# Optimization experiments

Measured on AMD Instinct MI355X. Metric: run time of the kernel, lower is better.

Reference implementation:

```python
import jax, jax.numpy as jnp
import numpy as np

N = 131072   # num_nodes
E = 262144   # events in the batch
D = 128      # memory_dim
R = 128      # raw_msg_dim
T = 32       # time_dim


def setup_inputs() -> dict:
    key = jax.random.key(0)
    ks = jax.random.split(key, 16)
    s = 0.05
    return {
        "memory": jax.random.normal(ks[0], (N, D), jnp.float32) * s,
        "raw_msg": jax.random.normal(ks[1], (E, R), jnp.float32) * s,
        "time_w": jax.random.normal(ks[2], (T,), jnp.float32) * s,
        "time_b": jax.random.normal(ks[3], (T,), jnp.float32) * s,
        "W_msg_s": jax.random.normal(ks[4], (D, 2 * D + R + T), jnp.float32) * s,
        "b_msg_s": jax.random.normal(ks[5], (D,), jnp.float32) * s,
        "W_msg_d": jax.random.normal(ks[6], (D, 2 * D + R + T), jnp.float32) * s,
        "b_msg_d": jax.random.normal(ks[7], (D,), jnp.float32) * s,
        "W_ih": jax.random.normal(ks[8], (3 * D, D), jnp.float32) * s,
        "W_hh": jax.random.normal(ks[9], (3 * D, D), jnp.float32) * s,
        "b_ih": jax.random.normal(ks[10], (3 * D,), jnp.float32) * s,
        "b_hh": jax.random.normal(ks[11], (3 * D,), jnp.float32) * s,
        "src": jax.random.randint(ks[12], (E,), 0, N, jnp.int32),
        "dst": jax.random.randint(ks[13], (E,), 0, N, jnp.int32),
        "t": jax.random.randint(ks[14], (E,), 0, 100000, jnp.int32),
        "last_update": jax.random.randint(ks[15], (N,), 0, 50000, jnp.int32),
    }


def _time_enc(t_rel, time_w, time_b):
    # TimeEncoder: cos(Linear(t)) ; t_rel: [E] float -> [E, T]
    return jnp.cos(t_rel[:, None] * time_w[None, :] + time_b[None, :])


def _message(mem_a, mem_b, raw_msg, t_enc, W, b):
    # message MLP on concat(mem_src, mem_dst, raw_msg, t_enc)
    x = jnp.concatenate([mem_a, mem_b, raw_msg, t_enc], axis=-1)  # [E, 2D+R+T]
    return jax.nn.relu(x @ W.T + b)


def _forward(memory, raw_msg, time_w, time_b, W_msg_s, b_msg_s, W_msg_d, b_msg_d,
             W_ih, W_hh, b_ih, b_hh, src, dst, t, last_update):
    tf = t.astype(jnp.float32)
    lu = last_update.astype(jnp.float32)
    mem_s = memory[src]  # gather [E, D]
    mem_d = memory[dst]

    # source-side messages (stored under key src): t_rel = t - last_update[src]
    t_enc_s = _time_enc(tf - lu[src], time_w, time_b)
    msg_s = _message(mem_s, mem_d, raw_msg, t_enc_s, W_msg_s, b_msg_s)
    # dest-side messages (stored under key dst, src/dst swapped)
    t_enc_d = _time_enc(tf - lu[dst], time_w, time_b)
    msg_d = _message(mem_d, mem_s, raw_msg, t_enc_d, W_msg_d, b_msg_d)

    # scatter mean-aggregate messages onto their owner node
    seg = jnp.concatenate([src, dst], axis=0)          # [2E]
    vals = jnp.concatenate([msg_s, msg_d], axis=0)     # [2E, D]
    sums = jax.ops.segment_sum(vals, seg, num_segments=N)
    cnt = jax.ops.segment_sum(jnp.ones((2 * E,), jnp.float32), seg, num_segments=N)
    aggr = sums / jnp.maximum(cnt, 1.0)[:, None]       # [N, D]

    # GRUCell(aggr, memory)
    gi = aggr @ W_ih.T + b_ih
    gh = memory @ W_hh.T + b_hh
    i_r, i_z, i_n = jnp.split(gi, 3, axis=-1)
    h_r, h_z, h_n = jnp.split(gh, 3, axis=-1)
    r = jax.nn.sigmoid(i_r + h_r)
    z = jax.nn.sigmoid(i_z + h_z)
    n = jnp.tanh(i_n + r * h_n)
    new_memory = (1.0 - z) * n + z * memory

    # scatter-max timestamps (pyg scatter reduce='max' fills empty slots with 0)
    tt = jnp.concatenate([t, t], axis=0)
    seg_max = jax.ops.segment_max(tt, seg, num_segments=N)
    new_last_update = jnp.where(cnt > 0, seg_max, jnp.zeros((), jnp.int32))
    return new_memory, new_last_update


def reference(memory, raw_msg, time_w, time_b, W_msg_s, b_msg_s, W_msg_d, b_msg_d,
              W_ih, W_hh, b_ih, b_hh, src, dst, t, last_update):
    return _forward(memory, raw_msg, time_w, time_b, W_msg_s, b_msg_s, W_msg_d,
                    b_msg_d, W_ih, W_hh, b_ih, b_hh, src, dst, t, last_update)
```

## Files before the change

### kernel.cpp

```cpp
#include <hip/hip_runtime.h>
#include <cstdint>
#include <cstddef>

#define NN 131072
#define EE 262144

typedef __attribute__((ext_vector_type(8))) short bf16x8;
typedef __attribute__((ext_vector_type(4))) float f32x4;

__device__ __forceinline__ unsigned short f2bf(float f) {
    unsigned int u = __builtin_bit_cast(unsigned int, f);
    u += 0x7FFFu + ((u >> 16) & 1u);
    return (unsigned short)(u >> 16);
}
__device__ __forceinline__ float bf2f(unsigned short s) {
    unsigned int u = ((unsigned int)s) << 16;
    return __builtin_bit_cast(float, u);
}
__device__ __forceinline__ float sigmoidf_(float x) { return 1.0f / (1.0f + __expf(-x)); }
__device__ __forceinline__ float tanhf_(float x) {
    float ax = fabsf(x);
    float e = __expf(-2.0f * ax);
    return copysignf((1.0f - e) / (1.0f + e), x);
}
__device__ __forceinline__ bf16x8 pack8(const float* f) {
    bf16x8 o;
#pragma unroll
    for (int i = 0; i < 8; ++i) o[i] = (short)f2bf(f[i]);
    return o;
}

__device__ __forceinline__ float wmsg_val(int n, int k, const float* Ws, const float* Wd) {
    if (n < 128) {
        return (k < 416) ? Ws[n * 416 + k] : 0.0f;
    } else {
        int m = n - 128;
        if (k < 128)       return Wd[m * 416 + 128 + k];
        else if (k < 256)  return Wd[m * 416 + (k - 128)];
        else if (k < 384)  return Wd[m * 416 + k];
        else if (k < 416)  return 0.0f;
        else               return Wd[m * 416 + 384 + (k - 416)];
    }
}
__device__ __forceinline__ float wgru_val(int j, int k, const float* Wih, const float* Whh) {
    if (j < 256)      return (k < 128) ? Wih[j * 128 + k] : Whh[j * 128 + (k - 128)];
    else if (j < 384) return (k < 128) ? Wih[j * 128 + k] : 0.0f;
    else              return (k < 128) ? 0.0f : Whh[(j - 128) * 128 + (k - 128)];
}

__global__ void k_prep_msgfrag(const float* __restrict__ Ws, const float* __restrict__ Wd,
                               const float* __restrict__ bs, const float* __restrict__ bd,
                               unsigned short* __restrict__ Wmf, float* __restrict__ bm) {
    int b = blockIdx.x;
    int c = b >> 4, nt = b & 15;
    int lane = threadIdx.x;
    int col0 = lane & 15, q = lane >> 4;
    int n = nt * 16 + col0;
    float f[8];
#pragma unroll
    for (int j = 0; j < 8; ++j) f[j] = wmsg_val(n, c * 32 + q * 8 + j, Ws, Wd);
    ((bf16x8*)Wmf)[(size_t)b * 64 + lane] = pack8(f);
    if (b == 0)
        for (int i = lane; i < 256; i += 64) bm[i] = (i < 128) ? bs[i] : bd[i - 128];
}

__global__ void k_prep_grufrag(const float* __restrict__ Wih, const float* __restrict__ Whh,
                               const float* __restrict__ bih, const float* __restrict__ bhh,
                               unsigned short* __restrict__ Wgf, float* __restrict__ bg) {
    int b = blockIdx.x;
    int c = b >> 5, nt = b & 31;
    int lane = threadIdx.x;
    int col0 = lane & 15, q = lane >> 4;
    int j0 = nt * 16 + col0;
    float f[8];
#pragma unroll
    for (int j = 0; j < 8; ++j) f[j] = wgru_val(j0, c * 32 + q * 8 + j, Wih, Whh);
    ((bf16x8*)Wgf)[(size_t)b * 64 + lane] = pack8(f);
    if (b == 0)
        for (int i = lane; i < 512; i += 64)
            bg[i] = (i < 256) ? (bih[i] + bhh[i]) : ((i < 384) ? bih[i] : bhh[i - 128]);
}

__global__ void k_memconv(const float* __restrict__ in, unsigned short* __restrict__ outp) {
    int gid = blockIdx.x * 256 + threadIdx.x;
    const float4 v = ((const float4*)in)[gid];
    ushort4 o;
    o.x = f2bf(v.x); o.y = f2bf(v.y); o.z = f2bf(v.z); o.w = f2bf(v.w);
    *(ushort4*)(outp + (size_t)gid * 4) = o;
}

__global__ void k_pre(const int* __restrict__ t, const int* __restrict__ src,
                      const int* __restrict__ dst, const int* __restrict__ lu,
                      float* __restrict__ trel_s, float* __restrict__ trel_d,
                      int* cnt, int* lu_tmp) {
    int e = blockIdx.x * 256 + threadIdx.x;
    int s = src[e], d = dst[e], tv = t[e];
    trel_s[e] = (float)(tv - lu[s]);
    trel_d[e] = (float)(tv - lu[d]);
    atomicAdd(&cnt[s], 1);
    atomicAdd(&cnt[d], 1);
    atomicMax(&lu_tmp[s], tv);
    atomicMax(&lu_tmp[d], tv);
}

__global__ void k_scan1(const int* __restrict__ cnt, int* __restrict__ bsum) {
    __shared__ int red[256];
    int tid = threadIdx.x;
    red[tid] = cnt[blockIdx.x * 256 + tid];
    __syncthreads();
    for (int s = 128; s > 0; s >>= 1) {
        if (tid < s) red[tid] += red[tid + s];
        __syncthreads();
    }
    if (tid == 0) bsum[blockIdx.x] = red[0];
}
__global__ void k_scan2(const int* __restrict__ bsum, int* __restrict__ boff) {
    __shared__ int sb[512];
    int tid = threadIdx.x;
    int v = bsum[tid];
    sb[tid] = v;
    __syncthreads();
    for (int d = 1; d < 512; d <<= 1) {
        int u = (tid >= d) ? sb[tid - d] : 0;
        __syncthreads();
        sb[tid] += u;
        __syncthreads();
    }
    boff[tid] = sb[tid] - v;
}
__global__ void k_scan3(const int* __restrict__ cnt, const int* __restrict__ boff,
                        int* __restrict__ off, int* __restrict__ cursor) {
    __shared__ int sb[256];
    int tid = threadIdx.x;
    int i = blockIdx.x * 256 + tid;
    int v = cnt[i];
    sb[tid] = v;
    __syncthreads();
    for (int d = 1; d < 256; d <<= 1) {
        int u = (tid >= d) ? sb[tid - d] : 0;
        __syncthreads();
        sb[tid] += u;
        __syncthreads();
    }
    int o = boff[blockIdx.x] + sb[tid] - v;
    off[i] = o;
    cursor[i] = o;
}
__global__ void k_fill(const int* __restrict__ src, const int* __restrict__ dst,
                       int* cursor, int* __restrict__ pos2) {
    int e2 = blockIdx.x * 256 + threadIdx.x;
    int node = (e2 < EE) ? src[e2] : dst[e2 - EE];
    pos2[e2] = atomicAdd(&cursor[node], 1);
}

__launch_bounds__(256, 3)
__global__ void k_msg(const unsigned short* __restrict__ memb,
                      const float* __restrict__ raw,
                      const float* __restrict__ trel_s,
                      const float* __restrict__ trel_d,
                      const unsigned short* __restrict__ Wmf,
                      const float* __restrict__ bm,
                      const int* __restrict__ src, const int* __restrict__ dst,
                      const int* __restrict__ pos2,
                      const float* __restrict__ tw, const float* __restrict__ tb,
                      unsigned short* __restrict__ msg) {
    __shared__ int s_idx[64], d_idx[64], s_pos[64], d_pos[64];
    __shared__ float s_tw[32], s_tb[32];
    __shared__ __align__(16) unsigned short As[2][64 * 40];

    const int tid = threadIdx.x;
    const int e0 = blockIdx.x * 64;
    if (tid < 64)        { s_idx[tid] = src[e0 + tid];            s_pos[tid] = pos2[e0 + tid]; }
    else if (tid < 128)  { d_idx[tid - 64] = dst[e0 + tid - 64];  d_pos[tid - 64] = pos2[EE + e0 + tid - 64]; }
    else if (tid < 160)  s_tw[tid - 128] = tw[tid - 128];
    else if (tid < 192)  s_tb[tid - 160] = tb[tid - 160];
    __syncthreads();

    const int lane = tid & 63, w = tid >> 6;
    const int col0 = lane & 15, q = lane >> 4;

    auto stage = [&](int cc) {
        unsigned short* A = As[cc & 1];
        if (cc < 8) {
            int row = tid >> 2, seg = tid & 3;
            int node = (cc < 4) ? s_idx[row] : d_idx[row];
            bf16x8 v = *(const bf16x8*)(memb + (size_t)node * 128 + (cc & 3) * 32 + seg * 8);
            *(bf16x8*)&A[row * 40 + seg * 8] = v;
        } else if (cc < 12) {
#pragma unroll
            for (int i = 0; i < 2; ++i) {
                int lin = tid + 256 * i;
                int row = lin >> 3, seg = lin & 7;
                const float4 v = *(const float4*)(raw + (size_t)(e0 + row) * 128 + (cc - 8) * 32 + seg * 4);
                ushort4 o;
                o.x = f2bf(v.x); o.y = f2bf(v.y); o.z = f2bf(v.z); o.w = f2bf(v.w);
                *(ushort4*)&A[row * 40 + seg * 4] = o;
            }
        } else {
            int row = tid >> 2, quarter = tid & 3;
            float tr = (cc == 12) ? trel_s[e0 + row] : trel_d[e0 + row];
            float f[8];
#pragma unroll
            for (int j2 = 0; j2 < 8; ++j2) {
                int jj = quarter * 8 + j2;
                f[j2] = __cosf(tr * s_tw[jj] + s_tb[jj]);
            }
            *(bf16x8*)&A[row * 40 + quarter * 8] = pack8(f);
        }
    };

    f32x4 acc[4][4];
#pragma unroll
    for (int a = 0; a < 4; ++a)
#pragma unroll
        for (int b = 0; b < 4; ++b)
#pragma unroll
            for (int i = 0; i < 4; ++i) acc[a][b][i] = 0.0f;

    stage(0);
    __syncthreads();

    for (int c = 0; c < 14; ++c) {
        bf16x8 bfr[4];
        const bf16x8* Wc = (const bf16x8*)Wmf + (size_t)c * 16 * 64;
#pragma unroll
        for (int nl = 0; nl < 4; ++nl)
            bfr[nl] = Wc[(w * 4 + nl) * 64 + lane];
        const unsigned short* A = As[c & 1];
        bf16x8 afr[4];
#pragma unroll
        for (int mt = 0; mt < 4; ++mt)
            afr[mt] = *(const bf16x8*)&A[(mt * 16 + col0) * 40 + q * 8];
        if (c < 13) stage(c + 1);
#pragma unroll
        for (int mt = 0; mt < 4; ++mt)
#pragma unroll
            for (int nl = 0; nl < 4; ++nl)
                acc[mt][nl] = __builtin_amdgcn_mfma_f32_16x16x32_bf16(afr[mt], bfr[nl], acc[mt][nl], 0, 0, 0);
        __syncthreads();
    }

    unsigned short* scr = &As[0][0] + w * 1280;
    const bool is_s = (w < 2);
#pragma unroll
    for (int mt = 0; mt < 4; ++mt) {
#pragma unroll
        for (int nl = 0; nl < 4; ++nl) {
            int j = (w * 4 + nl) * 16 + col0;
            float bv = bm[j];
            int gl = nl * 2 + (col0 >> 3);
            int ci = col0 & 7;
#pragma unroll
            for (int r = 0; r < 4; ++r) {
                int rr = q * 4 + r;
                float v = fmaxf(acc[mt][nl][r] + bv, 0.0f);
                scr[rr * 80 + ((gl + rr) & 7) * 8 + ci] = f2bf(v);
            }
        }
        asm volatile("s_waitcnt lgkmcnt(0)" ::: "memory");
        {
            int rr2 = lane & 15, p = lane >> 4;
            int ev = mt * 16 + rr2;
            int pos = is_s ? s_pos[ev] : d_pos[ev];
            bf16x8 v0 = *(const bf16x8*)&scr[rr2 * 80 + (((2 * p)     + rr2) & 7) * 8];
            bf16x8 v1 = *(const bf16x8*)&scr[rr2 * 80 + (((2 * p + 1) + rr2) & 7) * 8];
            unsigned short* dstp = msg + (size_t)pos * 128 + (w & 1) * 64 + p * 16;
            *(bf16x8*)dstp = v0;
            *(bf16x8*)(dstp + 8) = v1;
        }
        asm volatile("s_waitcnt lgkmcnt(0)" ::: "memory");
    }
}

__launch_bounds__(256, 3)
__global__ void k_gru(const unsigned short* __restrict__ msg,
                      const int* __restrict__ off, const int* __restrict__ cnt,
                      const float* __restrict__ memory,
                      const unsigned short* __restrict__ Wgf,
                      const float* __restrict__ bg,
                      float* __restrict__ out) {
    __shared__ __align__(16) unsigned short Xs[32 * 264];

    const int tid = threadIdx.x;
    const int n0 = blockIdx.x * 32;

    {
        int g = tid >> 3, sub = tid & 7;
        int node = n0 + g;
        int beg = off[node], cn = cnt[node];
        float a[16];
#pragma unroll
        for (int i = 0; i < 16; ++i) a[i] = 0.0f;
        for (int m = 0; m < cn; ++m) {
            const bf16x8* p = (const bf16x8*)(msg + (size_t)(beg + m) * 128 + sub * 16);
            bf16x8 v0 = p[0], v1 = p[1];
#pragma unroll
            for (int k = 0; k < 8; ++k) {
                a[k]     += bf2f((unsigned short)v0[k]);
                a[8 + k] += bf2f((unsigned short)v1[k]);
            }
        }
        float inv = 1.0f / (float)(cn > 1 ? cn : 1);
#pragma unroll
        for (int i = 0; i < 16; ++i) a[i] *= inv;
        *(bf16x8*)&Xs[g * 264 + sub * 16] = pack8(&a[0]);
        *(bf16x8*)&Xs[g * 264 + sub * 16 + 8] = pack8(&a[8]);
        float f[16];
        const float4* mp = (const float4*)(memory + (size_t)node * 128 + sub * 16);
#pragma unroll
        for (int s = 0; s < 4; ++s) {
            float4 v = mp[s];
            f[s * 4 + 0] = v.x; f[s * 4 + 1] = v.y; f[s * 4 + 2] = v.z; f[s * 4 + 3] = v.w;
        }
        *(bf16x8*)&Xs[g * 264 + 128 + sub * 16] = pack8(&f[0]);
        *(bf16x8*)&Xs[g * 264 + 128 + sub * 16 + 8] = pack8(&f[8]);
    }
    __syncthreads();

    const int lane = tid & 63, w = tid >> 6;
    const int col0 = lane & 15, q = lane >> 4;

    f32x4 acc[2][4][2];
#pragma unroll
    for (int a = 0; a < 2; ++a)
#pragma unroll
        for (int g = 0; g < 4; ++g)
#pragma unroll
            for (int f = 0; f < 2; ++f)
#pragma unroll
                for (int i = 0; i < 4; ++i) acc[a][g][f][i] = 0.0f;

#pragma unroll
    for (int c = 0; c < 8; ++c) {
        bf16x8 bfr[4][2];
        const bf16x8* Wc = (const bf16x8*)Wgf + (size_t)c * 32 * 64;
#pragma unroll
        for (int g = 0; g < 4; ++g)
#pragma unroll
            for (int fh = 0; fh < 2; ++fh)
                bfr[g][fh] = Wc[(8 * g + 2 * w + fh) * 64 + lane];
        bf16x8 afr[2];
#pragma unroll
        for (int mt = 0; mt < 2; ++mt)
            afr[mt] = *(const bf16x8*)&Xs[(mt * 16 + col0) * 264 + c * 32 + q * 8];
#pragma unroll
        for (int mt = 0; mt < 2; ++mt)
#pragma unroll
            for (int g = 0; g < 4; ++g)
#pragma unroll
                for (int fh = 0; fh < 2; ++fh)
                    acc[mt][g][fh] = __builtin_amdgcn_mfma_f32_16x16x32_bf16(afr[mt], bfr[g][fh], acc[mt][g][fh], 0, 0, 0);
    }

#pragma unroll
    for (int fh = 0; fh < 2; ++fh) {
        int feat = w * 32 + fh * 16 + col0;
        float b_r = bg[feat], b_z = bg[128 + feat], b_in = bg[256 + feat], b_hn = bg[384 + feat];
#pragma unroll
        for (int mt = 0; mt < 2; ++mt) {
#pragma unroll
            for (int r = 0; r < 4; ++r) {
                int node = n0 + mt * 16 + q * 4 + r;
                float rr = sigmoidf_(acc[mt][0][fh][r] + b_r);
                float zz = sigmoidf_(acc[mt][1][fh][r] + b_z);
                float nn = tanhf_((acc[mt][2][fh][r] + b_in) + rr * (acc[mt][3][fh][r] + b_hn));
                float h = memory[(size_t)node * 128 + feat];
                out[(size_t)node * 128 + feat] = (1.0f - zz) * nn + zz * h;
            }
        }
    }
}

__global__ void k_lu(const int* __restrict__ lu_tmp, float* __restrict__ outp) {
    int i = blockIdx.x * 256 + threadIdx.x;
    outp[i] = (float)lu_tmp[i];
}

extern "C" void kernel_launch(void* const* d_in, const int* in_sizes, int n_in,
                              void* d_out, int out_size, void* d_ws, size_t ws_size,
                              hipStream_t stream) {
    const float* memory = (const float*)d_in[0];
    const float* raw    = (const float*)d_in[1];
    const float* tw     = (const float*)d_in[2];
    const float* tb     = (const float*)d_in[3];
    const float* Wms    = (const float*)d_in[4];
    const float* bms    = (const float*)d_in[5];
    const float* Wmd    = (const float*)d_in[6];
    const float* bmd    = (const float*)d_in[7];
    const float* Wih    = (const float*)d_in[8];
    const float* Whh    = (const float*)d_in[9];
    const float* bih    = (const float*)d_in[10];
    const float* bhh    = (const float*)d_in[11];
    const int* src = (const int*)d_in[12];
    const int* dst = (const int*)d_in[13];
    const int* t   = (const int*)d_in[14];
    const int* lu  = (const int*)d_in[15];

    char* ws = (char*)d_ws;
    size_t ob = 0;
    unsigned short* memb = (unsigned short*)(ws + ob); ob += (size_t)NN * 128 * 2;
    unsigned short* msg  = (unsigned short*)(ws + ob); ob += (size_t)2 * EE * 128 * 2;
    float* trel_s        = (float*)(ws + ob);          ob += (size_t)EE * 4;
    float* trel_d        = (float*)(ws + ob);          ob += (size_t)EE * 4;
    int* cnt             = (int*)(ws + ob);            ob += (size_t)NN * 4;
    int* off             = (int*)(ws + ob);            ob += (size_t)NN * 4;
    int* cursor          = (int*)(ws + ob);            ob += (size_t)NN * 4;
    int* lu_tmp          = (int*)(ws + ob);            ob += (size_t)NN * 4;
    int* pos2            = (int*)(ws + ob);            ob += (size_t)2 * EE * 4;
    int* bsum            = (int*)(ws + ob);            ob += 512 * 4;
    int* boff            = (int*)(ws + ob);            ob += 512 * 4;
    unsigned short* Wmf  = (unsigned short*)(ws + ob); ob += (size_t)14 * 16 * 64 * 8 * 2;
    float* bm            = (float*)(ws + ob);          ob += 256 * 4;
    unsigned short* Wgf  = (unsigned short*)(ws + ob); ob += (size_t)8 * 32 * 64 * 8 * 2;
    float* bg            = (float*)(ws + ob);          ob += 512 * 4;

    float* out = (float*)d_out;

    hipMemsetAsync(cnt, 0, (size_t)NN * 4, stream);
    hipMemsetAsync(lu_tmp, 0, (size_t)NN * 4, stream);

    k_prep_msgfrag<<<14 * 16, 64, 0, stream>>>(Wms, Wmd, bms, bmd, Wmf, bm);
    k_prep_grufrag<<<8 * 32, 64, 0, stream>>>(Wih, Whh, bih, bhh, Wgf, bg);
    k_memconv<<<(NN * 128 / 4) / 256, 256, 0, stream>>>(memory, memb);
    k_pre<<<EE / 256, 256, 0, stream>>>(t, src, dst, lu, trel_s, trel_d, cnt, lu_tmp);
    k_scan1<<<512, 256, 0, stream>>>(cnt, bsum);
    k_scan2<<<1, 512, 0, stream>>>(bsum, boff);
    k_scan3<<<512, 256, 0, stream>>>(cnt, boff, off, cursor);
    k_fill<<<2 * EE / 256, 256, 0, stream>>>(src, dst, cursor, pos2);
    k_msg<<<EE / 64, 256, 0, stream>>>(memb, raw, trel_s, trel_d, Wmf, bm, src, dst, pos2, tw, tb, msg);
    k_gru<<<NN / 32, 256, 0, stream>>>(msg, off, cnt, memory, Wgf, bg, out);
    k_lu<<<NN / 256, 256, 0, stream>>>(lu_tmp, out + (size_t)NN * 128);
}
```

Before: 589.0 us.

## Restructure message GEMM staging into 64-wide K chunks with register prefetch

```diff
diff --git a/kernel.cpp b/kernel.cpp
--- a/kernel.cpp
+++ b/kernel.cpp
@@ -166,7 +166,7 @@
                       unsigned short* __restrict__ msg) {
     __shared__ int s_idx[64], d_idx[64], s_pos[64], d_pos[64];
     __shared__ float s_tw[32], s_tb[32];
-    __shared__ __align__(16) unsigned short As[2][64 * 40];
+    __shared__ __align__(16) unsigned short As[2][64 * 72];
 
     const int tid = threadIdx.x;
     const int e0 = blockIdx.x * 64;
@@ -179,33 +179,54 @@
     const int lane = tid & 63, w = tid >> 6;
     const int col0 = lane & 15, q = lane >> 4;
 
-    auto stage = [&](int cc) {
-        unsigned short* A = As[cc & 1];
-        if (cc < 8) {
-            int row = tid >> 2, seg = tid & 3;
-            int node = (cc < 4) ? s_idx[row] : d_idx[row];
-            bf16x8 v = *(const bf16x8*)(memb + (size_t)node * 128 + (cc & 3) * 32 + seg * 8);
-            *(bf16x8*)&A[row * 40 + seg * 8] = v;
-        } else if (cc < 12) {
-#pragma unroll
-            for (int i = 0; i < 2; ++i) {
-                int lin = tid + 256 * i;
-                int row = lin >> 3, seg = lin & 7;
-                const float4 v = *(const float4*)(raw + (size_t)(e0 + row) * 128 + (cc - 8) * 32 + seg * 4);
-                ushort4 o;
-                o.x = f2bf(v.x); o.y = f2bf(v.y); o.z = f2bf(v.z); o.w = f2bf(v.w);
-                *(ushort4*)&A[row * 40 + seg * 4] = o;
+    const int mrow0 = tid >> 3, mseg = tid & 7;
+    const int rrow  = tid >> 4, rseg = tid & 15;
+    const int trow  = tid >> 2, tq   = tid & 3;
+
+    float4 p0, p1, p2, p3;
+
+    auto stage_load = [&](int t) {
+        if (t < 4) {
+            int colb = (t & 1) * 64;
+            int n0i = (t < 2) ? s_idx[mrow0] : d_idx[mrow0];
+            int n1i = (t < 2) ? s_idx[mrow0 + 32] : d_idx[mrow0 + 32];
+            p0 = *(const float4*)(memb + (size_t)n0i * 128 + colb + mseg * 8);
+            p1 = *(const float4*)(memb + (size_t)n1i * 128 + colb + mseg * 8);
+        } else if (t < 6) {
+            const float* rbase = raw + (size_t)e0 * 128 + (t & 1) * 64 + rseg * 4;
+            p0 = *(const float4*)(rbase + (size_t)(rrow +  0) * 128);
+            p1 = *(const float4*)(rbase + (size_t)(rrow + 16) * 128);
+            p2 = *(const float4*)(rbase + (size_t)(rrow + 32) * 128);
+            p3 = *(const float4*)(rbase + (size_t)(rrow + 48) * 128);
+        } else {
+            p0.x = (tq < 2) ? trel_s[e0 + trow] : trel_d[e0 + trow];
+        }
+    };
+
+    auto stage_write = [&](int t, unsigned short* A) {
+        if (t < 4) {
+            *(bf16x8*)&A[mrow0 * 72 + mseg * 8]        = __builtin_bit_cast(bf16x8, p0);
+            *(bf16x8*)&A[(mrow0 + 32) * 72 + mseg * 8] = __builtin_bit_cast(bf16x8, p1);
+        } else if (t < 6) {
+            ushort4 o;
+            o.x = f2bf(p0.x); o.y = f2bf(p0.y); o.z = f2bf(p0.z); o.w = f2bf(p0.w);
+            *(ushort4*)&A[(rrow +  0) * 72 + rseg * 4] = o;
+            o.x = f2bf(p1.x); o.y = f2bf(p1.y); o.z = f2bf(p1.z); o.w = f2bf(p1.w);
+            *(ushort4*)&A[(rrow + 16) * 72 + rseg * 4] = o;
+            o.x = f2bf(p2.x); o.y = f2bf(p2.y); o.z = f2bf(p2.z); o.w = f2bf(p2.w);
+            *(ushort4*)&A[(rrow + 32) * 72 + rseg * 4] = o;
+            o.x = f2bf(p3.x); o.y = f2bf(p3.y); o.z = f2bf(p3.z); o.w = f2bf(p3.w);
+            *(ushort4*)&A[(rrow + 48) * 72 + rseg * 4] = o;
+        } else {
+            float f[16];
+            float tr = p0.x;
+#pragma unroll
+            for (int j = 0; j < 16; ++j) {
+                int jj = (tq & 1) * 16 + j;
+                f[j] = __cosf(tr * s_tw[jj] + s_tb[jj]);
             }
-        } else {
-            int row = tid >> 2, quarter = tid & 3;
-            float tr = (cc == 12) ? trel_s[e0 + row] : trel_d[e0 + row];
-            float f[8];
-#pragma unroll
-            for (int j2 = 0; j2 < 8; ++j2) {
-                int jj = quarter * 8 + j2;
-                f[j2] = __cosf(tr * s_tw[jj] + s_tb[jj]);
-            }
-            *(bf16x8*)&A[row * 40 + quarter * 8] = pack8(f);
+            *(bf16x8*)&A[trow * 72 + tq * 16]     = pack8(&f[0]);
+            *(bf16x8*)&A[trow * 72 + tq * 16 + 8] = pack8(&f[8]);
         }
     };
 
@@ -217,26 +238,33 @@
 #pragma unroll
             for (int i = 0; i < 4; ++i) acc[a][b][i] = 0.0f;
 
-    stage(0);
-    __syncthreads();
-
-    for (int c = 0; c < 14; ++c) {
-        bf16x8 bfr[4];
-        const bf16x8* Wc = (const bf16x8*)Wmf + (size_t)c * 16 * 64;
-#pragma unroll
-        for (int nl = 0; nl < 4; ++nl)
-            bfr[nl] = Wc[(w * 4 + nl) * 64 + lane];
-        const unsigned short* A = As[c & 1];
-        bf16x8 afr[4];
-#pragma unroll
-        for (int mt = 0; mt < 4; ++mt)
-            afr[mt] = *(const bf16x8*)&A[(mt * 16 + col0) * 40 + q * 8];
-        if (c < 13) stage(c + 1);
-#pragma unroll
-        for (int mt = 0; mt < 4; ++mt)
+    stage_load(0);
+    stage_write(0, As[0]);
+    stage_load(1);
+    __syncthreads();
+
+#pragma unroll
+    for (int t = 0; t < 7; ++t) {
+        unsigned short* A = As[t & 1];
+        if (t < 6) stage_write(t + 1, As[(t + 1) & 1]);
+        if (t < 5) stage_load(t + 2);
+#pragma unroll
+        for (int kk = 0; kk < 2; ++kk) {
+            bf16x8 bfr[4];
+            const bf16x8* Wc = (const bf16x8*)Wmf + (size_t)(2 * t + kk) * 16 * 64;
 #pragma unroll
             for (int nl = 0; nl < 4; ++nl)
-                acc[mt][nl] = __builtin_amdgcn_mfma_f32_16x16x32_bf16(afr[mt], bfr[nl], acc[mt][nl], 0, 0, 0);
+                bfr[nl] = Wc[(w * 4 + nl) * 64 + lane];
+            bf16x8 afr[4];
+#pragma unroll
+            for (int mt = 0; mt < 4; ++mt)
+                afr[mt] = *(const bf16x8*)&A[(mt * 16 + col0) * 72 + kk * 32 + q * 8];
+#pragma unroll
+            for (int mt = 0; mt < 4; ++mt)
+#pragma unroll
+                for (int nl = 0; nl < 4; ++nl)
+                    acc[mt][nl] = __builtin_amdgcn_mfma_f32_16x16x32_bf16(afr[mt], bfr[nl], acc[mt][nl], 0, 0, 0);
+        }
         __syncthreads();
     }
 
```

After: 566.6 us. 1.04x faster.
